# Kernel tuning notes

Hardware: AMD Instinct MI355X
Metric: run time of the kernel (lower is better)

The kernel has to match this reference:

```python
import jax, jax.numpy as jnp
import numpy as np

B, T, C = 2, 2048, 1024
NH = 16
HD = C // NH  # 64
FF = 4 * C
EPS = 1e-5


def layer_norm(x, w, b):
    mu = jnp.mean(x, axis=-1, keepdims=True)
    var = jnp.mean(jnp.square(x - mu), axis=-1, keepdims=True)
    return (x - mu) * jax.lax.rsqrt(var + EPS) * w + b


def setup_inputs() -> dict:
    key = jax.random.key(0)
    ks = jax.random.split(key, 12)
    s_in = 1.0 / np.sqrt(C)
    s_ff = 1.0 / np.sqrt(FF)
    return {
        "x": jax.random.normal(ks[0], (B, T, C), jnp.float32),
        "ln1_w": jnp.ones((C,), jnp.float32),
        "ln1_b": jnp.zeros((C,), jnp.float32),
        "Wq": jax.random.normal(ks[1], (C, C), jnp.float32) * s_in,
        "Wk": jax.random.normal(ks[2], (C, C), jnp.float32) * s_in,
        "Wv": jax.random.normal(ks[3], (C, C), jnp.float32) * s_in,
        "Wp": jax.random.normal(ks[4], (C, C), jnp.float32) * s_in,
        "bp": jnp.zeros((C,), jnp.float32),
        "ln2_w": jnp.ones((C,), jnp.float32),
        "ln2_b": jnp.zeros((C,), jnp.float32),
        "W1": jax.random.normal(ks[5], (C, FF), jnp.float32) * s_in,
        "b1": jnp.zeros((FF,), jnp.float32),
        "W2": jax.random.normal(ks[6], (FF, C), jnp.float32) * s_ff,
        "b2": jnp.zeros((C,), jnp.float32),
    }


def reference(x, ln1_w, ln1_b, Wq, Wk, Wv, Wp, bp, ln2_w, ln2_b, W1, b1, W2, b2):
    scale = HD ** (-0.5)
    h = layer_norm(x, ln1_w, ln1_b)  # [B,T,C]
    # project and split heads: [B,T,NH,HD] -> [B,NH,T,HD]
    q = (h @ Wq).reshape(B, T, NH, HD).transpose(0, 2, 1, 3)
    k = (h @ Wk).reshape(B, T, NH, HD).transpose(0, 2, 1, 3)
    v = (h @ Wv).reshape(B, T, NH, HD).transpose(0, 2, 1, 3)
    scores = jnp.einsum("bhqd,bhkd->bhqk", q, k) * scale  # [B,NH,T,T]
    causal = jnp.tril(jnp.ones((T, T), jnp.bool_))
    scores = jnp.where(causal, scores, -jnp.inf)
    attn = jax.nn.softmax(scores, axis=-1)
    o = jnp.einsum("bhqk,bhkd->bhqd", attn, v)  # [B,NH,T,HD]
    o = o.transpose(0, 2, 1, 3).reshape(B, T, C)
    x = x + o @ Wp + bp
    h2 = layer_norm(x, ln2_w, ln2_b)
    x = x + jax.nn.relu(h2 @ W1 + b1) @ W2 + b2
    return x
```

## Files before the change

kernel.cpp:

```cpp
#include <hip/hip_runtime.h>
#include <hip/hip_bf16.h>

using u16 = unsigned short;
typedef short v8s __attribute__((ext_vector_type(8)));
typedef float v4f __attribute__((ext_vector_type(4)));

#define B_ 2
#define T_ 2048
#define C_ 1024
#define NH_ 16
#define HD_ 64
#define FF_ 4096
#define NT (B_*T_)
#define QKVC 3072

__device__ __forceinline__ u16 f2b(float f) {
  union { float f; unsigned int i; } v; v.f = f;
  unsigned int r = (v.i + 0x7FFFu + ((v.i >> 16) & 1u)) >> 16;
  return (u16)r;
}
__device__ __forceinline__ v4f mfma16(v8s a, v8s b, v4f c) {
  return __builtin_amdgcn_mfma_f32_16x16x32_bf16(a, b, c, 0, 0, 0);
}
__device__ __forceinline__ void glds16(const u16* g, u16* l) {
  __builtin_amdgcn_global_load_lds(
      (const __attribute__((address_space(1))) unsigned int*)g,
      (__attribute__((address_space(3))) unsigned int*)l, 16, 0, 0);
}

__global__ __launch_bounds__(256) void wcvt_kernel(const float* __restrict__ W,
    u16* __restrict__ Wt, int K, int N) {
  __shared__ float t[32][33];
  int tx = threadIdx.x & 31, ty = threadIdx.x >> 5;
  int n0 = blockIdx.x * 32, k0 = blockIdx.y * 32;
#pragma unroll
  for (int j = 0; j < 4; ++j)
    t[ty + j * 8][tx] = W[(size_t)(k0 + ty + j * 8) * N + n0 + tx];
  __syncthreads();
#pragma unroll
  for (int j = 0; j < 4; ++j)
    Wt[(size_t)(n0 + ty + j * 8) * K + k0 + tx] = f2b(t[tx][ty + j * 8]);
}

__global__ __launch_bounds__(256) void ln_kernel(const float* __restrict__ x,
    const float* __restrict__ w, const float* __restrict__ b, u16* __restrict__ y) {
  int row = blockIdx.x;
  int tid = threadIdx.x;
  const float* xr = x + (size_t)row * C_;
  float4 f4 = *(const float4*)&xr[tid * 4];
  float f[4] = {f4.x, f4.y, f4.z, f4.w};
  float s1 = 0.f, s2 = 0.f;
#pragma unroll
  for (int i = 0; i < 4; ++i) { s1 += f[i]; s2 += f[i] * f[i]; }
#pragma unroll
  for (int off = 32; off > 0; off >>= 1) {
    s1 += __shfl_down(s1, off);
    s2 += __shfl_down(s2, off);
  }
  __shared__ float red[10];
  int lane = tid & 63, wid = tid >> 6;
  if (lane == 0) { red[wid] = s1; red[4 + wid] = s2; }
  __syncthreads();
  if (tid == 0) {
    float a = red[0] + red[1] + red[2] + red[3];
    float q = red[4] + red[5] + red[6] + red[7];
    float mu = a * (1.f / C_);
    float var = q * (1.f / C_) - mu * mu;
    red[8] = mu; red[9] = rsqrtf(var + 1e-5f);
  }
  __syncthreads();
  float mu = red[8], rs = red[9];
  union { uint2 v; u16 s[4]; } st;
#pragma unroll
  for (int i = 0; i < 4; ++i) {
    int c = tid * 4 + i;
    st.s[i] = f2b((f[i] - mu) * rs * w[c] + b[c]);
  }
  *(uint2*)&y[(size_t)row * C_ + tid * 4] = st.v;
}

__global__ __launch_bounds__(256) void gemm_bt(const u16* __restrict__ X,
    const u16* __restrict__ Wt, const float* __restrict__ bias,
    const float* __restrict__ resf, u16* __restrict__ Yb, float* __restrict__ Yf,
    float* __restrict__ Yfz1, int M, int N, int lda, int ldb, int kspl, int relu) {
  __shared__ __align__(16) u16 As[2][128 * 32];
  __shared__ __align__(16) u16 Bs[2][128 * 32];
  int tid = threadIdx.x, lane = tid & 63, w = tid >> 6;
  int wm = w >> 1, wn = w & 1, quad = lane >> 4, lcol = lane & 15;
  int m0 = blockIdx.y * 128, n0 = blockIdx.x * 128;
  int koff = blockIdx.z * kspl;
  v4f acc[4][4] = {};
  int sr = lane >> 2, sc = lane & 3;
  const u16* gA = X  + (size_t)(m0 + w * 32 + sr) * lda + koff + sc * 8;
  const u16* gB = Wt + (size_t)(n0 + w * 32 + sr) * ldb + koff + sc * 8;
  u16* lA0 = As[0] + (w * 32) * 32;
  u16* lA1 = As[1] + (w * 32) * 32;
  u16* lB0 = Bs[0] + (w * 32) * 32;
  u16* lB1 = Bs[1] + (w * 32) * 32;
  for (int k0 = 0; k0 < kspl; k0 += 64) {
    __syncthreads();
    glds16(gA + k0,                        lA0);
    glds16(gA + k0 + (size_t)16 * lda,     lA0 + 16 * 32);
    glds16(gA + k0 + 32,                   lA1);
    glds16(gA + k0 + 32 + (size_t)16 * lda, lA1 + 16 * 32);
    glds16(gB + k0,                        lB0);
    glds16(gB + k0 + (size_t)16 * ldb,     lB0 + 16 * 32);
    glds16(gB + k0 + 32,                   lB1);
    glds16(gB + k0 + 32 + (size_t)16 * ldb, lB1 + 16 * 32);
    __syncthreads();
#pragma unroll
    for (int kh = 0; kh < 2; ++kh) {
      v8s a[4], b[4];
#pragma unroll
      for (int i = 0; i < 4; ++i) {
        a[i] = *(v8s*)&As[kh][(wm * 64 + i * 16 + lcol) * 32 + quad * 8];
        b[i] = *(v8s*)&Bs[kh][(wn * 64 + i * 16 + lcol) * 32 + quad * 8];
      }
#pragma unroll
      for (int i = 0; i < 4; ++i)
#pragma unroll
        for (int j = 0; j < 4; ++j)
          acc[i][j] = mfma16(a[i], b[j], acc[i][j]);
    }
  }
  float* yf = blockIdx.z ? Yfz1 : Yf;
#pragma unroll
  for (int i = 0; i < 4; ++i) {
    int mb = m0 + wm * 64 + i * 16 + quad * 4;
#pragma unroll
    for (int j = 0; j < 4; ++j) {
      int n = n0 + wn * 64 + j * 16 + lcol;
#pragma unroll
      for (int r = 0; r < 4; ++r) {
        float v = acc[i][j][r];
        if (bias) v += bias[n];
        if (resf) v += resf[(size_t)(mb + r) * N + n];
        if (relu) v = fmaxf(v, 0.f);
        if (Yb) Yb[(size_t)(mb + r) * N + n] = f2b(v);
        else    yf[(size_t)(mb + r) * N + n] = v;
      }
    }
  }
}

__global__ __launch_bounds__(256) void gemm_bt_n64(const u16* __restrict__ X,
    const u16* __restrict__ Wt, const float* __restrict__ bias,
    const float* __restrict__ resf, u16* __restrict__ Yb, float* __restrict__ Yf,
    int M, int N, int K, int relu) {
  __shared__ __align__(16) u16 As[128 * 32];
  __shared__ __align__(16) u16 Bs[64 * 32];
  int tid = threadIdx.x, lane = tid & 63, w = tid >> 6;
  int wm = w >> 1, wn = w & 1, quad = lane >> 4, lcol = lane & 15;
  int m0 = blockIdx.y * 128, n0 = blockIdx.x * 64;
  v4f acc[4][2] = {};
  int sr = lane >> 2, sc = lane & 3;
  const u16* gA = X  + (size_t)(m0 + w * 32 + sr) * K + sc * 8;
  const u16* gB = Wt + (size_t)(n0 + w * 16 + sr) * K + sc * 8;
  u16* lA = As + (w * 32) * 32;
  u16* lB = Bs + (w * 16) * 32;
  for (int k0 = 0; k0 < K; k0 += 32) {
    __syncthreads();
    glds16(gA + k0, lA);
    glds16(gA + k0 + (size_t)16 * K, lA + 16 * 32);
    glds16(gB + k0, lB);
    __syncthreads();
    v8s a[4], b[2];
#pragma unroll
    for (int i = 0; i < 4; ++i)
      a[i] = *(v8s*)&As[(wm * 64 + i * 16 + lcol) * 32 + quad * 8];
#pragma unroll
    for (int j = 0; j < 2; ++j)
      b[j] = *(v8s*)&Bs[(wn * 32 + j * 16 + lcol) * 32 + quad * 8];
#pragma unroll
    for (int i = 0; i < 4; ++i)
#pragma unroll
      for (int j = 0; j < 2; ++j)
        acc[i][j] = mfma16(a[i], b[j], acc[i][j]);
  }
#pragma unroll
  for (int i = 0; i < 4; ++i) {
    int mb = m0 + wm * 64 + i * 16 + quad * 4;
#pragma unroll
    for (int j = 0; j < 2; ++j) {
      int n = n0 + wn * 32 + j * 16 + lcol;
#pragma unroll
      for (int r = 0; r < 4; ++r) {
        float v = acc[i][j][r];
        if (bias) v += bias[n];
        if (resf) v += resf[(size_t)(mb + r) * N + n];
        if (relu) v = fmaxf(v, 0.f);
        if (Yb) Yb[(size_t)(mb + r) * N + n] = f2b(v);
        else    Yf[(size_t)(mb + r) * N + n] = v;
      }
    }
  }
}

__global__ __launch_bounds__(256) void add4_kernel(float* __restrict__ out,
    const float* __restrict__ p0, const float* __restrict__ bias,
    const float* __restrict__ res) {
  size_t e0 = ((size_t)blockIdx.x * 256 + threadIdx.x) * 4;
  int col = (int)(e0 & (C_ - 1));
  float4 o = *(float4*)&out[e0];
  float4 p = *(const float4*)&p0[e0];
  float4 r = *(const float4*)&res[e0];
  float4 bb = *(const float4*)&bias[col];
  o.x += p.x + r.x + bb.x;
  o.y += p.y + r.y + bb.y;
  o.z += p.z + r.z + bb.z;
  o.w += p.w + r.w + bb.w;
  *(float4*)&out[e0] = o;
}

__global__ __launch_bounds__(256) void vt_kernel(const u16* __restrict__ QKV,
    u16* __restrict__ VT) {
  int bh = blockIdx.x, tt = blockIdx.y;
  int b = bh >> 4, h = bh & 15;
  int tid = threadIdx.x;
  __shared__ u16 L[64 * 72];
  int r = tid >> 2, g = tid & 3;
  size_t row = ((size_t)(b * T_ + tt * 64 + r)) * QKVC + 2 * C_ + h * HD_;
  union { uint4 v; u16 s[8]; } a0, a1;
  a0.v = *(const uint4*)&QKV[row + g * 8];
  a1.v = *(const uint4*)&QKV[row + 32 + g * 8];
#pragma unroll
  for (int e = 0; e < 8; ++e) L[(g * 8 + e) * 72 + r] = a0.s[e];
#pragma unroll
  for (int e = 0; e < 8; ++e) L[(32 + g * 8 + e) * 72 + r] = a1.s[e];
  __syncthreads();
  size_t orow = ((size_t)(bh * 64 + r)) * T_ + tt * 64;
  *(uint4*)&VT[orow + g * 8]      = *(uint4*)&L[r * 72 + g * 8];
  *(uint4*)&VT[orow + 32 + g * 8] = *(uint4*)&L[r * 72 + 32 + g * 8];
}

__global__ __launch_bounds__(256) void attn_kernel(const u16* __restrict__ QKV,
    const u16* __restrict__ VT, u16* __restrict__ Ob) {
  int bh = blockIdx.x, qt = blockIdx.y;
  int b = bh >> 4, h = bh & 15;
  int tid = threadIdx.x, lane = tid & 63, wid = tid >> 6;
  int quad = lane >> 4, lcol = lane & 15;
  __shared__ __align__(16) u16 Ps[4][32 * 72];
  const float SC = 0.125f * 1.44269504f;
  const float EB = 8.0f * 1.44269504f;
  int qg[2];
  v8s bq[2][2];
#pragma unroll
  for (int j = 0; j < 2; ++j) {
    qg[j] = qt * 128 + wid * 32 + j * 16 + lcol;
#pragma unroll
    for (int kh = 0; kh < 2; ++kh)
      bq[j][kh] = *(const v8s*)&QKV[(size_t)(b * T_ + qg[j]) * QKVC + h * HD_ + kh * 32 + quad * 8];
  }
  float l_i[2] = {0.f, 0.f};
  v4f accO[4][2] = {};
  int kbmax = 2 * qt + (wid >> 1);
  const u16* kbase = QKV + (size_t)b * T_ * QKVC + C_ + h * HD_;
  const u16* vbase = VT + (size_t)(bh * 64) * T_;
  for (int kb = 0; kb <= kbmax; ++kb) {
    v8s ak[4][2], av[4][2];
#pragma unroll
    for (int cg = 0; cg < 4; ++cg)
#pragma unroll
      for (int kh = 0; kh < 2; ++kh)
        ak[cg][kh] = *(const v8s*)&kbase[(size_t)(kb * 64 + cg * 16 + lcol) * QKVC + kh * 32 + quad * 8];
#pragma unroll
    for (int df = 0; df < 4; ++df)
#pragma unroll
      for (int kh = 0; kh < 2; ++kh)
        av[df][kh] = *(const v8s*)&vbase[(size_t)(df * 16 + lcol) * T_ + kb * 64 + kh * 32 + quad * 8];
    bool diag = (kb == kbmax);
#pragma unroll
    for (int j = 0; j < 2; ++j) {
      v4f s[4];
#pragma unroll
      for (int cg = 0; cg < 4; ++cg) {
        v4f acc = {};
        acc = mfma16(ak[cg][1], bq[j][1], acc);
        s[cg] = mfma16(ak[cg][0], bq[j][0], acc);
      }
      float ps = 0.f;
#pragma unroll
      for (int cg = 0; cg < 4; ++cg) {
        union { u16 s4[4]; unsigned long long ll; } pk;
#pragma unroll
        for (int rg = 0; rg < 4; ++rg) {
          float pv = exp2f(s[cg][rg] * SC - EB);
          if (diag) {
            int kt = kb * 64 + cg * 16 + quad * 4 + rg;
            pv = (kt <= qg[j]) ? pv : 0.f;
          }
          ps += pv;
          pk.s4[rg] = f2b(pv);
        }
        *(unsigned long long*)&Ps[wid][(j * 16 + lcol) * 72 + cg * 16 + quad * 4] = pk.ll;
      }
      ps += __shfl_xor(ps, 16);
      ps += __shfl_xor(ps, 32);
      l_i[j] += ps;
      v8s bp0 = *(v8s*)&Ps[wid][(j * 16 + lcol) * 72 + quad * 8];
      v8s bp1 = *(v8s*)&Ps[wid][(j * 16 + lcol) * 72 + 32 + quad * 8];
#pragma unroll
      for (int df = 0; df < 4; ++df) {
        v4f t = mfma16(av[df][1], bp1, accO[df][j]);
        accO[df][j] = mfma16(av[df][0], bp0, t);
      }
    }
  }
#pragma unroll
  for (int j = 0; j < 2; ++j) {
    float inv = 1.f / l_i[j];
    size_t orow = ((size_t)(b * T_ + qg[j])) * C_ + h * HD_;
#pragma unroll
    for (int df = 0; df < 4; ++df) {
      union { u16 s4[4]; unsigned long long ll; } ok;
#pragma unroll
      for (int rg = 0; rg < 4; ++rg) ok.s4[rg] = f2b(accO[df][j][rg] * inv);
      *(unsigned long long*)&Ob[orow + df * 16 + quad * 4] = ok.ll;
    }
  }
}

extern "C" void kernel_launch(void* const* d_in, const int* in_sizes, int n_in,
                              void* d_out, int out_size, void* d_ws, size_t ws_size,
                              hipStream_t stream) {
  (void)in_sizes; (void)n_in; (void)out_size; (void)ws_size;
  const float* x    = (const float*)d_in[0];
  const float* ln1w = (const float*)d_in[1];
  const float* ln1b = (const float*)d_in[2];
  const float* Wq   = (const float*)d_in[3];
  const float* Wk   = (const float*)d_in[4];
  const float* Wv   = (const float*)d_in[5];
  const float* Wp   = (const float*)d_in[6];
  const float* bp   = (const float*)d_in[7];
  const float* ln2w = (const float*)d_in[8];
  const float* ln2b = (const float*)d_in[9];
  const float* W1   = (const float*)d_in[10];
  const float* b1   = (const float*)d_in[11];
  const float* W2   = (const float*)d_in[12];
  const float* b2   = (const float*)d_in[13];
  float* out = (float*)d_out;
  char* ws = (char*)d_ws;
  const size_t MB = 1024 * 1024;
  u16*   h1    = (u16*)(ws);
  u16*   VT    = (u16*)(ws);
  u16*   QKVb  = (u16*)(ws + 8  * MB);
  u16*   Ob    = (u16*)(ws + 32 * MB);
  float* xa    = (float*)(ws + 40 * MB);
  u16*   h2    = (u16*)(ws);
  u16*   f1    = (u16*)(ws + 8 * MB);
  u16*   Wqkvt = (u16*)(ws + 56 * MB);
  u16*   Wpt   = (u16*)(ws + 62 * MB);
  u16*   W1t   = (u16*)(ws + 64 * MB);
  u16*   W2t   = (u16*)(ws + 72 * MB);
  float* p0    = (float*)(ws + 56 * MB);

  wcvt_kernel<<<dim3(32, 32),  256, 0, stream>>>(Wq, Wqkvt,                1024, 1024);
  wcvt_kernel<<<dim3(32, 32),  256, 0, stream>>>(Wk, Wqkvt + 1024 * 1024,  1024, 1024);
  wcvt_kernel<<<dim3(32, 32),  256, 0, stream>>>(Wv, Wqkvt + 2048 * 1024,  1024, 1024);
  wcvt_kernel<<<dim3(32, 32),  256, 0, stream>>>(Wp, Wpt,                  1024, 1024);
  wcvt_kernel<<<dim3(128, 32), 256, 0, stream>>>(W1, W1t,                  1024, 4096);
  wcvt_kernel<<<dim3(32, 128), 256, 0, stream>>>(W2, W2t,                  4096, 1024);

  ln_kernel<<<NT, 256, 0, stream>>>(x, ln1w, ln1b, h1);
  gemm_bt<<<dim3(QKVC / 128, NT / 128, 1), 256, 0, stream>>>(
      h1, Wqkvt, nullptr, nullptr, QKVb, nullptr, nullptr, NT, QKVC, C_, C_, C_, 0);
  vt_kernel<<<dim3(B_ * NH_, T_ / 64), 256, 0, stream>>>(QKVb, VT);
  attn_kernel<<<dim3(B_ * NH_, T_ / 128), 256, 0, stream>>>(QKVb, VT, Ob);
  gemm_bt_n64<<<dim3(C_ / 64, NT / 128), 256, 0, stream>>>(
      Ob, Wpt, bp, x, nullptr, xa, NT, C_, C_, 0);
  ln_kernel<<<NT, 256, 0, stream>>>(xa, ln2w, ln2b, h2);
  gemm_bt<<<dim3(FF_ / 128, NT / 128, 1), 256, 0, stream>>>(
      h2, W1t, b1, nullptr, f1, nullptr, nullptr, NT, FF_, C_, C_, C_, 1);
  gemm_bt<<<dim3(C_ / 128, NT / 128, 2), 256, 0, stream>>>(
      f1, W2t, nullptr, nullptr, nullptr, p0, out, NT, C_, FF_, FF_, FF_ / 2, 0);
  add4_kernel<<<(NT * C_) / (256 * 4), 256, 0, stream>>>(out, p0, b2, xa);
}
```

Baseline: 457.6 us.

## Pair causal query tiles per block and double-buffer K fragment loads

Each attention block now handles two query tiles, y and 15-y, so every block does roughly the same amount of causal work and the grid is halved. The K-tile register loads are double-buffered, so the next K block is fetched while the current tile is computed. This evens out block durations and hides global load latency, at the cost of more registers, possibly lower occupancy, and fewer blocks in flight (256 instead of 512).

```diff
diff --git a/kernel.cpp b/kernel.cpp
--- a/kernel.cpp
+++ b/kernel.cpp
@@ -235,87 +235,107 @@
 
 __global__ __launch_bounds__(256) void attn_kernel(const u16* __restrict__ QKV,
     const u16* __restrict__ VT, u16* __restrict__ Ob) {
-  int bh = blockIdx.x, qt = blockIdx.y;
+  int bh = blockIdx.x, y = blockIdx.y;
   int b = bh >> 4, h = bh & 15;
   int tid = threadIdx.x, lane = tid & 63, wid = tid >> 6;
   int quad = lane >> 4, lcol = lane & 15;
   __shared__ __align__(16) u16 Ps[4][32 * 72];
   const float SC = 0.125f * 1.44269504f;
   const float EB = 8.0f * 1.44269504f;
-  int qg[2];
-  v8s bq[2][2];
-#pragma unroll
-  for (int j = 0; j < 2; ++j) {
-    qg[j] = qt * 128 + wid * 32 + j * 16 + lcol;
-#pragma unroll
-    for (int kh = 0; kh < 2; ++kh)
-      bq[j][kh] = *(const v8s*)&QKV[(size_t)(b * T_ + qg[j]) * QKVC + h * HD_ + kh * 32 + quad * 8];
-  }
-  float l_i[2] = {0.f, 0.f};
-  v4f accO[4][2] = {};
-  int kbmax = 2 * qt + (wid >> 1);
   const u16* kbase = QKV + (size_t)b * T_ * QKVC + C_ + h * HD_;
   const u16* vbase = VT + (size_t)(bh * 64) * T_;
-  for (int kb = 0; kb <= kbmax; ++kb) {
-    v8s ak[4][2], av[4][2];
+  u16* psw = Ps[wid];
+
+  auto ldk = [&](v8s (&ak)[4][2], int kb) {
 #pragma unroll
     for (int cg = 0; cg < 4; ++cg)
 #pragma unroll
       for (int kh = 0; kh < 2; ++kh)
         ak[cg][kh] = *(const v8s*)&kbase[(size_t)(kb * 64 + cg * 16 + lcol) * QKVC + kh * 32 + quad * 8];
-#pragma unroll
-    for (int df = 0; df < 4; ++df)
+  };
+
+#pragma unroll
+  for (int pi = 0; pi < 2; ++pi) {
+    int qt = pi ? (15 - y) : y;
+    int qg[2];
+    v8s bq[2][2];
+#pragma unroll
+    for (int j = 0; j < 2; ++j) {
+      qg[j] = qt * 128 + wid * 32 + j * 16 + lcol;
 #pragma unroll
       for (int kh = 0; kh < 2; ++kh)
-        av[df][kh] = *(const v8s*)&vbase[(size_t)(df * 16 + lcol) * T_ + kb * 64 + kh * 32 + quad * 8];
-    bool diag = (kb == kbmax);
+        bq[j][kh] = *(const v8s*)&QKV[(size_t)(b * T_ + qg[j]) * QKVC + h * HD_ + kh * 32 + quad * 8];
+    }
+    float l_i[2] = {0.f, 0.f};
+    v4f accO[4][2] = {};
+    int kbmax = 2 * qt + (wid >> 1);
+
+    auto ctile = [&](v8s (&ak)[4][2], int kb, bool diag) {
+      v8s av[4][2];
+#pragma unroll
+      for (int df = 0; df < 4; ++df)
+#pragma unroll
+        for (int kh = 0; kh < 2; ++kh)
+          av[df][kh] = *(const v8s*)&vbase[(size_t)(df * 16 + lcol) * T_ + kb * 64 + kh * 32 + quad * 8];
+#pragma unroll
+      for (int j = 0; j < 2; ++j) {
+        v4f s[4];
+#pragma unroll
+        for (int cg = 0; cg < 4; ++cg) {
+          v4f acc = {};
+          acc = mfma16(ak[cg][1], bq[j][1], acc);
+          s[cg] = mfma16(ak[cg][0], bq[j][0], acc);
+        }
+        float ps = 0.f;
+#pragma unroll
+        for (int cg = 0; cg < 4; ++cg) {
+          union { u16 s4[4]; unsigned long long ll; } pk;
+#pragma unroll
+          for (int rg = 0; rg < 4; ++rg) {
+            float pv = exp2f(s[cg][rg] * SC - EB);
+            if (diag) {
+              int kt = kb * 64 + cg * 16 + quad * 4 + rg;
+              pv = (kt <= qg[j]) ? pv : 0.f;
+            }
+            ps += pv;
+            pk.s4[rg] = f2b(pv);
+          }
+          *(unsigned long long*)&psw[(j * 16 + lcol) * 72 + cg * 16 + quad * 4] = pk.ll;
+        }
+        ps += __shfl_xor(ps, 16);
+        ps += __shfl_xor(ps, 32);
+        l_i[j] += ps;
+        v8s bp0 = *(v8s*)&psw[(j * 16 + lcol) * 72 + quad * 8];
+        v8s bp1 = *(v8s*)&psw[(j * 16 + lcol) * 72 + 32 + quad * 8];
+#pragma unroll
+        for (int df = 0; df < 4; ++df) {
+          v4f t = mfma16(av[df][1], bp1, accO[df][j]);
+          accO[df][j] = mfma16(av[df][0], bp0, t);
+        }
+      }
+    };
+
+    v8s a0k[4][2], a1k[4][2];
+    ldk(a0k, 0);
+    for (int kb = 0; kb <= kbmax; kb += 2) {
+      if (kb + 1 <= kbmax) ldk(a1k, kb + 1);
+      ctile(a0k, kb, kb == kbmax);
+      if (kb + 1 <= kbmax) {
+        if (kb + 2 <= kbmax) ldk(a0k, kb + 2);
+        ctile(a1k, kb + 1, (kb + 1) == kbmax);
+      }
+    }
 #pragma unroll
     for (int j = 0; j < 2; ++j) {
-      v4f s[4];
-#pragma unroll
-      for (int cg = 0; cg < 4; ++cg) {
-        v4f acc = {};
-        acc = mfma16(ak[cg][1], bq[j][1], acc);
-        s[cg] = mfma16(ak[cg][0], bq[j][0], acc);
-      }
-      float ps = 0.f;
-#pragma unroll
-      for (int cg = 0; cg < 4; ++cg) {
-        union { u16 s4[4]; unsigned long long ll; } pk;
-#pragma unroll
-        for (int rg = 0; rg < 4; ++rg) {
-          float pv = exp2f(s[cg][rg] * SC - EB);
-          if (diag) {
-            int kt = kb * 64 + cg * 16 + quad * 4 + rg;
-            pv = (kt <= qg[j]) ? pv : 0.f;
-          }
-          ps += pv;
-          pk.s4[rg] = f2b(pv);
-        }
-        *(unsigned long long*)&Ps[wid][(j * 16 + lcol) * 72 + cg * 16 + quad * 4] = pk.ll;
-      }
-      ps += __shfl_xor(ps, 16);
-      ps += __shfl_xor(ps, 32);
-      l_i[j] += ps;
-      v8s bp0 = *(v8s*)&Ps[wid][(j * 16 + lcol) * 72 + quad * 8];
-      v8s bp1 = *(v8s*)&Ps[wid][(j * 16 + lcol) * 72 + 32 + quad * 8];
+      float inv = 1.f / l_i[j];
+      size_t orow = ((size_t)(b * T_ + qg[j])) * C_ + h * HD_;
 #pragma unroll
       for (int df = 0; df < 4; ++df) {
-        v4f t = mfma16(av[df][1], bp1, accO[df][j]);
-        accO[df][j] = mfma16(av[df][0], bp0, t);
-      }
-    }
-  }
-#pragma unroll
-  for (int j = 0; j < 2; ++j) {
-    float inv = 1.f / l_i[j];
-    size_t orow = ((size_t)(b * T_ + qg[j])) * C_ + h * HD_;
-#pragma unroll
-    for (int df = 0; df < 4; ++df) {
-      union { u16 s4[4]; unsigned long long ll; } ok;
-#pragma unroll
-      for (int rg = 0; rg < 4; ++rg) ok.s4[rg] = f2b(accO[df][j][rg] * inv);
-      *(unsigned long long*)&Ob[orow + df * 16 + quad * 4] = ok.ll;
+        union { u16 s4[4]; unsigned long long ll; } ok;
+#pragma unroll
+        for (int rg = 0; rg < 4; ++rg) ok.s4[rg] = f2b(accO[df][j][rg] * inv);
+        *(unsigned long long*)&Ob[orow + df * 16 + quad * 4] = ok.ll;
+      }
     }
   }
 }
@@ -365,7 +385,7 @@
   gemm_bt<<<dim3(QKVC / 128, NT / 128, 1), 256, 0, stream>>>(
       h1, Wqkvt, nullptr, nullptr, QKVb, nullptr, nullptr, NT, QKVC, C_, C_, C_, 0);
   vt_kernel<<<dim3(B_ * NH_, T_ / 64), 256, 0, stream>>>(QKVb, VT);
-  attn_kernel<<<dim3(B_ * NH_, T_ / 128), 256, 0, stream>>>(QKVb, VT, Ob);
+  attn_kernel<<<dim3(B_ * NH_, T_ / 256), 256, 0, stream>>>(QKVb, VT, Ob);
   gemm_bt_n64<<<dim3(C_ / 64, NT / 128), 256, 0, stream>>>(
       Ob, Wpt, bp, x, nullptr, xa, NT, C_, C_, 0);
   ln_kernel<<<NT, 256, 0, stream>>>(xa, ln2w, ln2b, h2);
```

New measurement: 445.9 us. -2.6%, faster.
